# Optimization experiments

Hardware: AMD Instinct MI355X
Metric: run time of the kernel (lower is better)

## Reference

```python
import jax, jax.numpy as jnp
import numpy as np

WD, WH, WW = 2, 7, 7
N = WD * WH * WW            # 98 tokens per window
C = 192                     # dim
H = 6                       # num_heads
HD = C // H                 # head_dim = 32
NW = 512                    # number of windows per sample
B = 4                       # batch
B_ = B * NW                 # 2048 windows total
TABLE = (2 * WD - 1) * (2 * WH - 1) * (2 * WW - 1)  # 507


def _relative_position_index():
    d, h, w = np.meshgrid(np.arange(WD), np.arange(WH), np.arange(WW), indexing='ij')
    coords = np.stack([d, h, w]).reshape(3, -1)              # (3, N)
    rel = coords[:, :, None] - coords[:, None, :]            # (3, N, N)
    rel = rel.transpose(1, 2, 0).astype(np.int64)            # (N, N, 3)
    rel[:, :, 0] += WD - 1
    rel[:, :, 1] += WH - 1
    rel[:, :, 2] += WW - 1
    rel[:, :, 0] *= (2 * WH - 1) * (2 * WW - 1)
    rel[:, :, 1] *= 2 * WW - 1
    return jnp.asarray(rel.sum(-1), dtype=jnp.int32)         # (N, N)


def setup_inputs() -> dict:
    key = jax.random.key(0)
    ks = jax.random.split(key, 7)
    return {
        'x': jax.random.normal(ks[0], (B_, N, C), dtype=jnp.float32),
        'mask': jax.random.normal(ks[1], (NW, N, N), dtype=jnp.float32),
        'qkv_w': jax.random.normal(ks[2], (3 * C, C), dtype=jnp.float32) * 0.02,
        'qkv_b': jnp.zeros((3 * C,), dtype=jnp.float32),
        'proj_w': jax.random.normal(ks[3], (C, C), dtype=jnp.float32) * 0.02,
        'proj_b': jnp.zeros((C,), dtype=jnp.float32),
        'rpb_table': jax.random.normal(ks[4], (TABLE, H), dtype=jnp.float32) * 0.02,
        'rel_pos_index': _relative_position_index(),
    }


def reference(x, mask, qkv_w, qkv_b, proj_w, proj_b, rpb_table, rel_pos_index):
    Bw, n, c = x.shape
    hd = c // H
    scale = hd ** -0.5
    qkv = (x @ qkv_w.T + qkv_b).reshape(Bw, n, 3, H, hd)
    q, k, v = qkv[:, :, 0], qkv[:, :, 1], qkv[:, :, 2]       # (Bw, n, H, hd)
    # attn = (q @ k^T) * scale  (scale applied after matmul, as in source)
    attn = jnp.einsum('bihd,bjhd->bhij', q, k) * scale       # (Bw, H, n, n)
    bias = rpb_table[rel_pos_index]                          # (n, n, H)
    attn = attn + jnp.transpose(bias, (2, 0, 1))[None]       # broadcast over Bw
    nw = mask.shape[0]
    attn = attn.reshape(Bw // nw, nw, H, n, n) + mask[None, :, None]
    attn = jax.nn.softmax(attn.reshape(Bw, H, n, n), axis=-1)
    out = jnp.einsum('bhij,bjhd->bihd', attn, v).reshape(Bw, n, c)
    return out @ proj_w.T + proj_b
```

## Files before the change

### kernel.cpp

```cpp
#include <hip/hip_runtime.h>
#include <hip/hip_bf16.h>

using bf16   = __bf16;
using bf16x4 = __attribute__((ext_vector_type(4))) __bf16;
using bf16x8 = __attribute__((ext_vector_type(8))) __bf16;
using f32x4  = __attribute__((ext_vector_type(4))) float;

#define B_TOT 2048
#define NTOK  98
#define CDIM  192
#define NHEAD 6
#define HDIM  32
#define NWIN  512
#define NN    (NTOK*NTOK)
#define QKV_ELEMS ((size_t)B_TOT*NHEAD*NTOK*HDIM)
#define MROWS 200704
#define SCALE 0.17677669529663687f

#define MFMA(a,b,c) __builtin_amdgcn_mfma_f32_16x16x32_bf16((a),(b),(c),0,0,0)

#define GLD16(gp, lp) __builtin_amdgcn_global_load_lds(                        \
    (const __attribute__((address_space(1))) void*)(gp),                       \
    (__attribute__((address_space(3))) void*)(lp), 16, 0, 0)

__global__ void build_bias(const float* __restrict__ table,
                           const int* __restrict__ rel,
                           float* __restrict__ bias) {
    int t = blockIdx.x * 256 + threadIdx.x;
    if (t < NN) {
        int idx = rel[t];
        #pragma unroll
        for (int h = 0; h < NHEAD; ++h)
            bias[h * NN + t] = table[idx * NHEAD + h];
    }
}

__global__ void conv_swz(const float* __restrict__ src, bf16* __restrict__ dst,
                         int nchunk) {
    int t = blockIdx.x * 256 + threadIdx.x;
    if (t < nchunk) {
        int row = t / 24, c = t % 24;
        const float* s = src + (size_t)row * CDIM + c * 8;
        bf16x8 o;
        #pragma unroll
        for (int e = 0; e < 8; ++e) o[e] = (bf16)s[e];
        *(bf16x8*)(dst + (size_t)row * CDIM + ((c ^ (row & 7)) << 3)) = o;
    }
}

__global__ __launch_bounds__(256) void qkv_gemm(
    const float* __restrict__ x, const bf16* __restrict__ wb,
    const float* __restrict__ bvec,
    bf16* __restrict__ qdst, bf16* __restrict__ kdst, bf16* __restrict__ vdst)
{
    __shared__ char Bs[2][24576];
    const int tid = threadIdx.x, lane = tid & 63, wv = tid >> 6;
    const int l15 = lane & 15, l16 = lane >> 4;
    const int m0 = blockIdx.x * 64;

    {
        const char* bsrc = (const char*)wb;
        #pragma unroll
        for (int j = 0; j < 6; ++j) {
            const int ch = wv * 6 + j;
            GLD16(bsrc + ch * 1024 + lane * 16, Bs[0] + ch * 1024);
        }
    }

    const int arow = wv * 16 + l15;
    const int grow = m0 + arow;
    const float* xr = x + (size_t)grow * CDIM + l16 * 8;
    bf16x8 af[6];
    #pragma unroll
    for (int ks = 0; ks < 6; ++ks) {
        float4 v0 = *(const float4*)(xr + ks * 32);
        float4 v1 = *(const float4*)(xr + ks * 32 + 4);
        bf16x8 a;
        a[0] = (bf16)v0.x; a[1] = (bf16)v0.y; a[2] = (bf16)v0.z; a[3] = (bf16)v0.w;
        a[4] = (bf16)v1.x; a[5] = (bf16)v1.y; a[6] = (bf16)v1.z; a[7] = (bf16)v1.w;
        af[ks] = a;
    }

    __syncthreads();

    const int rowoff = (grow / NTOK) * 18816 + (grow % NTOK) * 32;
    const f32x4 z4 = {0.f, 0.f, 0.f, 0.f};

    #pragma unroll
    for (int nc = 0; nc < 9; ++nc) {
        if (nc < 8) {
            const char* bsrc = (const char*)wb + (size_t)(nc + 1) * 24576;
            #pragma unroll
            for (int j = 0; j < 6; ++j) {
                const int ch = wv * 6 + j;
                GLD16(bsrc + ch * 1024 + lane * 16, Bs[(nc + 1) & 1] + ch * 1024);
            }
        }

        f32x4 acc[4];
        #pragma unroll
        for (int ct = 0; ct < 4; ++ct) acc[ct] = z4;

        #pragma unroll
        for (int ks = 0; ks < 6; ++ks) {
            #pragma unroll
            for (int ct = 0; ct < 4; ++ct) {
                const int brow = ct * 16 + l15;
                bf16x8 bf = *(const bf16x8*)(Bs[nc & 1] + brow * 384
                                             + (((ks * 4 + l16) ^ (brow & 7)) << 4));
                acc[ct] = MFMA(bf, af[ks], acc[ct]);
            }
        }

        #pragma unroll
        for (int ct = 0; ct < 4; ++ct) {
            const int g0    = nc * 64 + ct * 16;
            const int which = g0 / CDIM;
            const int cm    = g0 % CDIM;
            const int h     = cm >> 5, hd0 = cm & 31;
            const float4 bvf = *(const float4*)(bvec + g0 + l16 * 4);
            bf16x4 s;
            #pragma unroll
            for (int r = 0; r < 4; ++r) {
                float v = acc[ct][r] + ((const float*)&bvf)[r];
                if (which == 0) v *= SCALE;
                s[r] = (bf16)v;
            }
            bf16* dp = (which == 0) ? qdst : (which == 1) ? kdst : vdst;
            *(bf16x4*)(dp + rowoff + h * 3136 + hd0 + l16 * 4) = s;
        }
        __syncthreads();
    }
}

__global__ __launch_bounds__(448) void attn_fused(
    const bf16* __restrict__ q, const bf16* __restrict__ k,
    const bf16* __restrict__ v,
    const float* __restrict__ mask, const float* __restrict__ bias,
    bf16* __restrict__ ao)
{
    __shared__ char lds[8192 + 28672 + 512];
    char* Vt = lds;
    char* P  = lds + 8192;
    float* invS = (float*)(lds + 8192 + 28672);

    const int bid = blockIdx.x;
    const int bh  = (bid & 7) * 1536 + (bid >> 3);
    const int b = bh / NHEAD, h = bh % NHEAD;
    const int w = b & (NWIN - 1);
    const int tid = threadIdx.x, lane = tid & 63, it = tid >> 6;
    const int l15 = lane & 15, l16 = lane >> 4;

    const size_t bho = (size_t)bh * 3136;
    if (tid < 392) {
        int n = tid >> 2, hd0 = (tid & 3) * 8;
        bf16x8 vv = *(const bf16x8*)(v + bho + n * 32 + hd0);
        #pragma unroll
        for (int e = 0; e < 8; ++e) {
            int hd = hd0 + e;
            *(bf16*)(Vt + hd * 256 + (((n >> 3) ^ (hd & 7)) << 4) + ((n & 7) << 1)) = vv[e];
        }
    }
    for (int f = tid; f < 32 * 30; f += 448) {
        int hd = f / 30, n = 98 + f % 30;
        *(bf16*)(Vt + hd * 256 + (((n >> 3) ^ (hd & 7)) << 4) + ((n & 7) << 1)) = (bf16)0.f;
    }
    {
        int zr = it * 16 + l15;
        int zc = 112 + l16 * 4;
        *(unsigned long long*)(P + zr * 256 + (((zc >> 3) ^ (zr & 7)) << 4) + ((zc & 7) << 1)) = 0ull;
    }

    int qrow = it * 16 + l15; if (qrow > 97) qrow = 97;
    const bf16* qsrc = q + bho;
    const bf16* ksrc = k + bho;
    const bf16x8 qf = *(const bf16x8*)(qsrc + qrow * HDIM + l16 * 8);
    const f32x4 z4 = {0.f, 0.f, 0.f, 0.f};
    f32x4 acc[7];
    #pragma unroll
    for (int jt = 0; jt < 7; ++jt) {
        int kr = jt * 16 + l15; if (kr > 97) kr = 97;
        bf16x8 kf = *(const bf16x8*)(ksrc + kr * HDIM + l16 * 8);
        acc[jt] = MFMA(qf, kf, z4);
    }

    const float* mrow = mask + (size_t)w * NN;
    const float* brow = bias + (size_t)h * NN;
    #pragma unroll
    for (int r = 0; r < 4; ++r) {
        const int iact = it * 16 + l16 * 4 + r;
        int i = iact > 97 ? 97 : iact;
        #pragma unroll
        for (int jt = 0; jt < 7; ++jt) {
            int j = jt * 16 + l15;
            acc[jt][r] = (j < NTOK)
                ? (acc[jt][r] + mrow[i * NTOK + j] + brow[i * NTOK + j])
                : -__builtin_inff();
        }
        float m = acc[0][r];
        #pragma unroll
        for (int jt = 1; jt < 7; ++jt) m = fmaxf(m, acc[jt][r]);
        m = fmaxf(m, __shfl_xor(m, 1, 16));
        m = fmaxf(m, __shfl_xor(m, 2, 16));
        m = fmaxf(m, __shfl_xor(m, 4, 16));
        m = fmaxf(m, __shfl_xor(m, 8, 16));
        float s = 0.f;
        #pragma unroll
        for (int jt = 0; jt < 7; ++jt) {
            float e = __expf(acc[jt][r] - m);
            acc[jt][r] = e; s += e;
        }
        s += __shfl_xor(s, 1, 16);
        s += __shfl_xor(s, 2, 16);
        s += __shfl_xor(s, 4, 16);
        s += __shfl_xor(s, 8, 16);
        if (l15 == 0) invS[iact] = 1.f / s;
    }

    #pragma unroll
    for (int jt = 0; jt < 7; ++jt) {
        #pragma unroll
        for (int r = 0; r < 4; ++r) {
            int row = it * 16 + l16 * 4 + r;
            int j = jt * 16 + l15;
            *(bf16*)(P + row * 256 + (((j >> 3) ^ (row & 7)) << 4) + ((j & 7) << 1))
                = (bf16)acc[jt][r];
        }
    }
    __syncthreads();

    f32x4 o0 = z4, o1 = z4;
    const int prow = it * 16 + l15;
    #pragma unroll
    for (int ks = 0; ks < 4; ++ks) {
        int kchunk = ks * 4 + l16;
        bf16x8 pf = *(const bf16x8*)(P + prow * 256 + ((kchunk ^ (prow & 7)) << 4));
        bf16x8 v0 = *(const bf16x8*)(Vt + l15 * 256 + ((kchunk ^ (l15 & 7)) << 4));
        bf16x8 v1 = *(const bf16x8*)(Vt + (16 + l15) * 256 + ((kchunk ^ (l15 & 7)) << 4));
        o0 = MFMA(v0, pf, o0);
        o1 = MFMA(v1, pf, o1);
    }

    {
        int row = it * 16 + l15;
        if (row < NTOK) {
            float inv = invS[row];
            bf16* dst = ao + (size_t)b * NTOK * CDIM;
            bf16x4 s0, s1;
            #pragma unroll
            for (int r = 0; r < 4; ++r) {
                s0[r] = (bf16)(o0[r] * inv);
                s1[r] = (bf16)(o1[r] * inv);
            }
            const int swr = (b * NTOK + row) & 7;
            const int c0 = h * 4 + (l16 >> 1);
            const int c1 = c0 + 2;
            const int wi = (l16 & 1) << 2;
            *(bf16x4*)(dst + (size_t)row * CDIM + (((c0 ^ swr) << 3) | wi)) = s0;
            *(bf16x4*)(dst + (size_t)row * CDIM + (((c1 ^ swr) << 3) | wi)) = s1;
        }
    }
}

__global__ __launch_bounds__(256) void proj_gemm(
    const bf16* __restrict__ ao, const bf16* __restrict__ wb,
    const float* __restrict__ bvec, float* __restrict__ out)
{
    __shared__ char As[24576];
    __shared__ char Bs[2][24576];
    const int tid = threadIdx.x, lane = tid & 63, wv = tid >> 6;
    const int l15 = lane & 15, l16 = lane >> 4;
    const int m0 = blockIdx.x * 64;

    {
        const char* asrc = (const char*)ao + (size_t)m0 * 384;
        const char* bsrc = (const char*)wb;
        #pragma unroll
        for (int j = 0; j < 6; ++j) {
            const int ch = wv * 6 + j;
            GLD16(asrc + ch * 1024 + lane * 16, As + ch * 1024);
            GLD16(bsrc + ch * 1024 + lane * 16, Bs[0] + ch * 1024);
        }
    }
    __syncthreads();

    const int arow = wv * 16 + l15;
    bf16x8 af[6];
    #pragma unroll
    for (int ks = 0; ks < 6; ++ks)
        af[ks] = *(const bf16x8*)(As + arow * 384 + (((ks * 4 + l16) ^ (arow & 7)) << 4));

    const size_t orow = (size_t)(m0 + arow) * CDIM;
    const f32x4 z4 = {0.f, 0.f, 0.f, 0.f};

    #pragma unroll
    for (int nc = 0; nc < 3; ++nc) {
        if (nc < 2) {
            const char* bsrc = (const char*)wb + (size_t)(nc + 1) * 24576;
            #pragma unroll
            for (int j = 0; j < 6; ++j) {
                const int ch = wv * 6 + j;
                GLD16(bsrc + ch * 1024 + lane * 16, Bs[(nc + 1) & 1] + ch * 1024);
            }
        }

        f32x4 acc[4];
        #pragma unroll
        for (int ct = 0; ct < 4; ++ct) acc[ct] = z4;

        #pragma unroll
        for (int ks = 0; ks < 6; ++ks) {
            #pragma unroll
            for (int ct = 0; ct < 4; ++ct) {
                const int brow = ct * 16 + l15;
                bf16x8 bf = *(const bf16x8*)(Bs[nc & 1] + brow * 384
                                             + (((ks * 4 + l16) ^ (brow & 7)) << 4));
                acc[ct] = MFMA(bf, af[ks], acc[ct]);
            }
        }

        #pragma unroll
        for (int ct = 0; ct < 4; ++ct) {
            const int g0 = nc * 64 + ct * 16;
            const float4 bvf = *(const float4*)(bvec + g0 + l16 * 4);
            f32x4 s;
            #pragma unroll
            for (int r = 0; r < 4; ++r)
                s[r] = acc[ct][r] + ((const float*)&bvf)[r];
            *(f32x4*)(out + orow + g0 + l16 * 4) = s;
        }
        __syncthreads();
    }
}

extern "C" void kernel_launch(void* const* d_in, const int* in_sizes, int n_in,
                              void* d_out, int out_size, void* d_ws, size_t ws_size,
                              hipStream_t stream)
{
    (void)in_sizes; (void)n_in; (void)out_size; (void)ws_size;
    const float* x      = (const float*)d_in[0];
    const float* mask   = (const float*)d_in[1];
    const float* qkv_w  = (const float*)d_in[2];
    const float* qkv_b  = (const float*)d_in[3];
    const float* proj_w = (const float*)d_in[4];
    const float* proj_b = (const float*)d_in[5];
    const float* rpb    = (const float*)d_in[6];
    const int*   rel    = (const int*)d_in[7];
    float* out = (float*)d_out;

    char* ws = (char*)d_ws;
    bf16* qb = (bf16*)ws;
    bf16* kb = qb + QKV_ELEMS;
    bf16* vb = kb + QKV_ELEMS;
    size_t off = 3 * QKV_ELEMS * sizeof(bf16);
    float* bias = (float*)(ws + off);
    off += ((size_t)NHEAD * NN * 4 + 255) / 256 * 256;
    bf16* ao = (bf16*)(ws + off);
    bf16* qwb = ao;
    bf16* pwb = qb;

    build_bias<<<(NN + 255) / 256, 256, 0, stream>>>(rpb, rel, bias);
    conv_swz<<<(576 * 24 + 255) / 256, 256, 0, stream>>>(qkv_w, qwb, 576 * 24);
    qkv_gemm<<<MROWS / 64, 256, 0, stream>>>(x, qwb, qkv_b, qb, kb, vb);
    attn_fused<<<B_TOT * NHEAD, 448, 0, stream>>>(qb, kb, vb, mask, bias, ao);
    conv_swz<<<(192 * 24 + 255) / 256, 256, 0, stream>>>(proj_w, pwb, 192 * 24);
    proj_gemm<<<MROWS / 64, 256, 0, stream>>>(ao, pwb, proj_b, out);
}
```

Before: 342.7 us.

## Reuse mask+bias registers across the batch by looping four windows per block

Each attention block now handles one (window, head) pair for all four batch samples. It loads the summed mask and relative-position bias into registers once and reuses them across four sequential iterations, instead of re-reading fp32 mask and bias from global memory for every batch element. The grid shrinks to a quarter of its former size and each block runs a serial loop with extra syncs, which lowers parallelism and latency hiding. Holding the mask+bias values in registers also raises register pressure.

```diff
diff --git a/kernel.cpp b/kernel.cpp
--- a/kernel.cpp
+++ b/kernel.cpp
@@ -145,22 +145,11 @@
     float* invS = (float*)(lds + 8192 + 28672);
 
     const int bid = blockIdx.x;
-    const int bh  = (bid & 7) * 1536 + (bid >> 3);
-    const int b = bh / NHEAD, h = bh % NHEAD;
-    const int w = b & (NWIN - 1);
+    const int wh  = (bid & 7) * 384 + (bid >> 3);
+    const int w = wh / NHEAD, h = wh % NHEAD;
     const int tid = threadIdx.x, lane = tid & 63, it = tid >> 6;
     const int l15 = lane & 15, l16 = lane >> 4;
 
-    const size_t bho = (size_t)bh * 3136;
-    if (tid < 392) {
-        int n = tid >> 2, hd0 = (tid & 3) * 8;
-        bf16x8 vv = *(const bf16x8*)(v + bho + n * 32 + hd0);
-        #pragma unroll
-        for (int e = 0; e < 8; ++e) {
-            int hd = hd0 + e;
-            *(bf16*)(Vt + hd * 256 + (((n >> 3) ^ (hd & 7)) << 4) + ((n & 7) << 1)) = vv[e];
-        }
-    }
     for (int f = tid; f < 32 * 30; f += 448) {
         int hd = f / 30, n = 98 + f % 30;
         *(bf16*)(Vt + hd * 256 + (((n >> 3) ^ (hd & 7)) << 4) + ((n & 7) << 1)) = (bf16)0.f;
@@ -171,94 +160,120 @@
         *(unsigned long long*)(P + zr * 256 + (((zc >> 3) ^ (zr & 7)) << 4) + ((zc & 7) << 1)) = 0ull;
     }
 
-    int qrow = it * 16 + l15; if (qrow > 97) qrow = 97;
-    const bf16* qsrc = q + bho;
-    const bf16* ksrc = k + bho;
-    const bf16x8 qf = *(const bf16x8*)(qsrc + qrow * HDIM + l16 * 8);
-    const f32x4 z4 = {0.f, 0.f, 0.f, 0.f};
-    f32x4 acc[7];
-    #pragma unroll
-    for (int jt = 0; jt < 7; ++jt) {
-        int kr = jt * 16 + l15; if (kr > 97) kr = 97;
-        bf16x8 kf = *(const bf16x8*)(ksrc + kr * HDIM + l16 * 8);
-        acc[jt] = MFMA(qf, kf, z4);
-    }
-
     const float* mrow = mask + (size_t)w * NN;
     const float* brow = bias + (size_t)h * NN;
+    f32x4 mb[7];
+    int irow[4];
     #pragma unroll
     for (int r = 0; r < 4; ++r) {
-        const int iact = it * 16 + l16 * 4 + r;
-        int i = iact > 97 ? 97 : iact;
+        int i = it * 16 + l16 * 4 + r; if (i > 97) i = 97;
+        irow[r] = i;
         #pragma unroll
         for (int jt = 0; jt < 7; ++jt) {
             int j = jt * 16 + l15;
-            acc[jt][r] = (j < NTOK)
-                ? (acc[jt][r] + mrow[i * NTOK + j] + brow[i * NTOK + j])
-                : -__builtin_inff();
-        }
-        float m = acc[0][r];
-        #pragma unroll
-        for (int jt = 1; jt < 7; ++jt) m = fmaxf(m, acc[jt][r]);
-        m = fmaxf(m, __shfl_xor(m, 1, 16));
-        m = fmaxf(m, __shfl_xor(m, 2, 16));
-        m = fmaxf(m, __shfl_xor(m, 4, 16));
-        m = fmaxf(m, __shfl_xor(m, 8, 16));
-        float s = 0.f;
+            mb[jt][r] = (j < NTOK) ? (mrow[i * NTOK + j] + brow[i * NTOK + j])
+                                   : -__builtin_inff();
+        }
+    }
+
+    int qrow = it * 16 + l15; if (qrow > 97) qrow = 97;
+    const f32x4 z4 = {0.f, 0.f, 0.f, 0.f};
+
+    #pragma unroll 1
+    for (int rep = 0; rep < 4; ++rep) {
+        const int b = rep * NWIN + w;
+        const size_t bho = (size_t)(b * NHEAD + h) * 3136;
+
+        if (tid < 392) {
+            int n = tid >> 2, hd0 = (tid & 3) * 8;
+            bf16x8 vv = *(const bf16x8*)(v + bho + n * 32 + hd0);
+            #pragma unroll
+            for (int e = 0; e < 8; ++e) {
+                int hd = hd0 + e;
+                *(bf16*)(Vt + hd * 256 + (((n >> 3) ^ (hd & 7)) << 4) + ((n & 7) << 1)) = vv[e];
+            }
+        }
+
+        const bf16* qsrc = q + bho;
+        const bf16* ksrc = k + bho;
+        const bf16x8 qf = *(const bf16x8*)(qsrc + qrow * HDIM + l16 * 8);
+        f32x4 acc[7];
         #pragma unroll
         for (int jt = 0; jt < 7; ++jt) {
-            float e = __expf(acc[jt][r] - m);
-            acc[jt][r] = e; s += e;
-        }
-        s += __shfl_xor(s, 1, 16);
-        s += __shfl_xor(s, 2, 16);
-        s += __shfl_xor(s, 4, 16);
-        s += __shfl_xor(s, 8, 16);
-        if (l15 == 0) invS[iact] = 1.f / s;
-    }
-
-    #pragma unroll
-    for (int jt = 0; jt < 7; ++jt) {
+            int kr = jt * 16 + l15; if (kr > 97) kr = 97;
+            bf16x8 kf = *(const bf16x8*)(ksrc + kr * HDIM + l16 * 8);
+            acc[jt] = MFMA(qf, kf, z4);
+        }
+
         #pragma unroll
         for (int r = 0; r < 4; ++r) {
-            int row = it * 16 + l16 * 4 + r;
-            int j = jt * 16 + l15;
-            *(bf16*)(P + row * 256 + (((j >> 3) ^ (row & 7)) << 4) + ((j & 7) << 1))
-                = (bf16)acc[jt][r];
-        }
-    }
-    __syncthreads();
-
-    f32x4 o0 = z4, o1 = z4;
-    const int prow = it * 16 + l15;
-    #pragma unroll
-    for (int ks = 0; ks < 4; ++ks) {
-        int kchunk = ks * 4 + l16;
-        bf16x8 pf = *(const bf16x8*)(P + prow * 256 + ((kchunk ^ (prow & 7)) << 4));
-        bf16x8 v0 = *(const bf16x8*)(Vt + l15 * 256 + ((kchunk ^ (l15 & 7)) << 4));
-        bf16x8 v1 = *(const bf16x8*)(Vt + (16 + l15) * 256 + ((kchunk ^ (l15 & 7)) << 4));
-        o0 = MFMA(v0, pf, o0);
-        o1 = MFMA(v1, pf, o1);
-    }
-
-    {
-        int row = it * 16 + l15;
-        if (row < NTOK) {
-            float inv = invS[row];
-            bf16* dst = ao + (size_t)b * NTOK * CDIM;
-            bf16x4 s0, s1;
+            #pragma unroll
+            for (int jt = 0; jt < 7; ++jt)
+                acc[jt][r] = acc[jt][r] + mb[jt][r];
+            float m = fmaxf(fmaxf(acc[0][r], acc[1][r]),
+                            fmaxf(acc[2][r], acc[3][r]));
+            m = fmaxf(m, fmaxf(fmaxf(acc[4][r], acc[5][r]), acc[6][r]));
+            m = fmaxf(m, __shfl_xor(m, 1, 16));
+            m = fmaxf(m, __shfl_xor(m, 2, 16));
+            m = fmaxf(m, __shfl_xor(m, 4, 16));
+            m = fmaxf(m, __shfl_xor(m, 8, 16));
+            float s = 0.f;
+            #pragma unroll
+            for (int jt = 0; jt < 7; ++jt) {
+                float e = __expf(acc[jt][r] - m);
+                acc[jt][r] = e; s += e;
+            }
+            s += __shfl_xor(s, 1, 16);
+            s += __shfl_xor(s, 2, 16);
+            s += __shfl_xor(s, 4, 16);
+            s += __shfl_xor(s, 8, 16);
+            if (l15 == 0) invS[it * 16 + l16 * 4 + r] = 1.f / s;
+        }
+
+        #pragma unroll
+        for (int jt = 0; jt < 7; ++jt) {
             #pragma unroll
             for (int r = 0; r < 4; ++r) {
-                s0[r] = (bf16)(o0[r] * inv);
-                s1[r] = (bf16)(o1[r] * inv);
-            }
-            const int swr = (b * NTOK + row) & 7;
-            const int c0 = h * 4 + (l16 >> 1);
-            const int c1 = c0 + 2;
-            const int wi = (l16 & 1) << 2;
-            *(bf16x4*)(dst + (size_t)row * CDIM + (((c0 ^ swr) << 3) | wi)) = s0;
-            *(bf16x4*)(dst + (size_t)row * CDIM + (((c1 ^ swr) << 3) | wi)) = s1;
-        }
+                int row = it * 16 + l16 * 4 + r;
+                int j = jt * 16 + l15;
+                *(bf16*)(P + row * 256 + (((j >> 3) ^ (row & 7)) << 4) + ((j & 7) << 1))
+                    = (bf16)acc[jt][r];
+            }
+        }
+        __syncthreads();
+
+        f32x4 o0 = z4, o1 = z4;
+        const int prow = it * 16 + l15;
+        #pragma unroll
+        for (int ks = 0; ks < 4; ++ks) {
+            int kchunk = ks * 4 + l16;
+            bf16x8 pf = *(const bf16x8*)(P + prow * 256 + ((kchunk ^ (prow & 7)) << 4));
+            bf16x8 v0 = *(const bf16x8*)(Vt + l15 * 256 + ((kchunk ^ (l15 & 7)) << 4));
+            bf16x8 v1 = *(const bf16x8*)(Vt + (16 + l15) * 256 + ((kchunk ^ (l15 & 7)) << 4));
+            o0 = MFMA(v0, pf, o0);
+            o1 = MFMA(v1, pf, o1);
+        }
+
+        {
+            int row = it * 16 + l15;
+            if (row < NTOK) {
+                float inv = invS[row];
+                bf16* dst = ao + (size_t)b * NTOK * CDIM;
+                bf16x4 s0, s1;
+                #pragma unroll
+                for (int r = 0; r < 4; ++r) {
+                    s0[r] = (bf16)(o0[r] * inv);
+                    s1[r] = (bf16)(o1[r] * inv);
+                }
+                const int swr = (b * NTOK + row) & 7;
+                const int c0 = h * 4 + (l16 >> 1);
+                const int c1 = c0 + 2;
+                const int wi = (l16 & 1) << 2;
+                *(bf16x4*)(dst + (size_t)row * CDIM + (((c0 ^ swr) << 3) | wi)) = s0;
+                *(bf16x4*)(dst + (size_t)row * CDIM + (((c1 ^ swr) << 3) | wi)) = s1;
+            }
+        }
+        if (rep < 3) __syncthreads();
     }
 }
 
@@ -362,7 +377,7 @@
     build_bias<<<(NN + 255) / 256, 256, 0, stream>>>(rpb, rel, bias);
     conv_swz<<<(576 * 24 + 255) / 256, 256, 0, stream>>>(qkv_w, qwb, 576 * 24);
     qkv_gemm<<<MROWS / 64, 256, 0, stream>>>(x, qwb, qkv_b, qb, kb, vb);
-    attn_fused<<<B_TOT * NHEAD, 448, 0, stream>>>(qb, kb, vb, mask, bias, ao);
+    attn_fused<<<NWIN * NHEAD, 448, 0, stream>>>(qb, kb, vb, mask, bias, ao);
     conv_swz<<<(192 * 24 + 255) / 256, 256, 0, stream>>>(proj_w, pwb, 192 * 24);
     proj_gemm<<<MROWS / 64, 256, 0, stream>>>(ao, pwb, proj_b, out);
 }
```

Result: no change. 346.5 us (+1.1%).
